# Optimization experiments

Measured on AMD Instinct MI355X. Metric: run time of the kernel, lower is better.

## Reference

```python
import jax, jax.numpy as jnp
import numpy as np

B, T, F, H = 16, 1024, 1024, 16
D = F // H  # 64

def setup_inputs() -> dict:
    key = jax.random.key(0)
    k0, k1, k2 = jax.random.split(key, 3)
    return {
        "x": jax.random.normal(k0, (B, T, F), jnp.float32),
        "mask": jnp.zeros((B, 1, T, 1), jnp.float32),
        "W_attn": jax.random.normal(k1, (F, 3 * F), jnp.float32) * 0.02,
        "b_attn": jnp.zeros((3 * F,), jnp.float32),
        "W_proj": jax.random.normal(k2, (F, F), jnp.float32) * 0.02,
        "b_proj": jnp.zeros((F,), jnp.float32),
    }

def reference(x, mask, W_attn, b_attn, W_proj, b_proj):
    # qkv projection (Conv1D == linear with transposed weight layout)
    qkv = x @ W_attn + b_attn                       # [B,T,3F]
    q, k, v = jnp.split(qkv, 3, axis=-1)
    split = lambda t: t.reshape(B, T, H, D).transpose(0, 2, 1, 3)  # [B,H,T,D]
    q, k, v = split(q), split(k), split(v)
    # non-standard: contract over T -> [B,H,D,D] score matrix
    s = jnp.einsum('bhtd,bhte->bhde', q, k) / jnp.sqrt(jnp.float32(D))
    tril = jnp.tril(jnp.ones((D, D), bool))         # bias buffer sliced to DxD
    s = jnp.where(tril, s, jnp.float32(-10000.0))
    # second matmul with V (before softmax), scaled by dk^2
    w = jnp.einsum('bhde,bhte->bhtd', s, v) / (jnp.float32(D) ** 2)  # [B,H,T,D]
    w = jax.nn.softmax(w + mask, axis=-2)           # softmax over T (dim=-2)
    a = w * v                                        # elementwise, not weighted sum
    merge = lambda t: t.transpose(0, 2, 1, 3).reshape(B, T, F)
    a = merge(a) @ W_proj + b_proj                   # output projection
    return a, merge(w)
```

## Files before the change

kernel.cpp:

```cpp
#include <hip/hip_runtime.h>
#include <math.h>

namespace {
constexpr int B = 16, T = 1024, F = 1024, H = 16, D = 64;
constexpr int NT = B * T;
constexpr int QKV_COLS = 3 * F;

constexpr size_t XHI_OFF = 0;
constexpr size_t XLO_OFF = 33554432;
constexpr size_t WAH_OFF = 67108864;
constexpr size_t WVL_OFF = 73400320;
constexpr size_t QB_OFF  = 75497472;
constexpr size_t KB_OFF  = 109051904;
constexpr size_t SB_OFF  = 142606336;
constexpr size_t AB_OFF  = 146800640;
constexpr size_t WPB_OFF = 180355072;
constexpr size_t VB_OFF   = QB_OFF;
constexpr size_t WRAW_OFF = XHI_OFF;
constexpr size_t SP_OFF   = WVL_OFF;
}

typedef __attribute__((ext_vector_type(8))) __bf16 bf16x8;
typedef __attribute__((ext_vector_type(4))) float f32x4;

__device__ __forceinline__ unsigned short f2bf(float f) {
  unsigned u = __builtin_bit_cast(unsigned, f);
  u += 0x7FFFu + ((u >> 16) & 1u);
  return (unsigned short)(u >> 16);
}
__device__ __forceinline__ float bf2f(unsigned short s) {
  return __builtin_bit_cast(float, (unsigned)s << 16);
}
__device__ __forceinline__ void gld16(const unsigned short* g, unsigned short* l) {
  __builtin_amdgcn_global_load_lds(
      (const __attribute__((address_space(1))) unsigned int*)g,
      (__attribute__((address_space(3))) unsigned int*)l, 16, 0, 0);
}

__global__ __launch_bounds__(256) void cast_x(const float* __restrict__ x,
                                              unsigned short* __restrict__ xhi,
                                              unsigned short* __restrict__ xlo) {
  int i = (blockIdx.x * 256 + threadIdx.x) * 4;
  float4 v = *(const float4*)&x[i];
  ushort4 h, l;
  h.x = f2bf(v.x); l.x = f2bf(v.x - bf2f(h.x));
  h.y = f2bf(v.y); l.y = f2bf(v.y - bf2f(h.y));
  h.z = f2bf(v.z); l.z = f2bf(v.z - bf2f(h.z));
  h.w = f2bf(v.w); l.w = f2bf(v.w - bf2f(h.w));
  *(ushort4*)&xhi[i] = h;
  *(ushort4*)&xlo[i] = l;
}

__global__ __launch_bounds__(256) void tcast(const float* __restrict__ W,
                                             unsigned short* __restrict__ Wt,
                                             unsigned short* __restrict__ Wlo,
                                             int ncols, int locol0) {
  __shared__ float tile[64][65];
  const int bx = blockIdx.x, by = blockIdx.y, tid = threadIdx.x;
#pragma unroll
  for (int i = 0; i < 16; ++i) {
    int idx = tid + i * 256;
    int r = idx >> 6, c = idx & 63;
    tile[r][c] = W[(size_t)(by * 64 + r) * ncols + bx * 64 + c];
  }
  __syncthreads();
#pragma unroll
  for (int i = 0; i < 16; ++i) {
    int idx = tid + i * 256;
    int r = idx >> 6, c = idx & 63;
    int col = bx * 64 + r;
    float w = tile[c][r];
    unsigned short h = f2bf(w);
    Wt[(size_t)col * 1024 + by * 64 + c] = h;
    if (col >= locol0) {
      Wlo[(size_t)(col - locol0) * 1024 + by * 64 + c] = f2bf(w - bf2f(h));
    }
  }
}

__device__ __forceinline__ void stage256(const unsigned short* __restrict__ Ag,
                                         const unsigned short* __restrict__ Bg,
                                         int row0, int col0, int kin,
                                         unsigned short* lbase, int wave,
                                         int lane) {
  const int rsub = lane >> 3;
  const int logb = ((lane & 7) ^ rsub) << 4;
  const int isB = logb >> 6;
  const int koff = kin + ((logb & 63) >> 1);
#pragma unroll
  for (int L = 0; L < 4; ++L) {
    const int R0 = (L * 8 + wave) * 8;
    const int r = R0 + rsub;
    const unsigned short* src =
        isB ? (Bg + (size_t)(col0 + r) * 1024 + koff)
            : (Ag + (size_t)(row0 + r) * 1024 + koff);
    gld16(src, lbase + (size_t)R0 * 64);
  }
}

template <int MODE>
__device__ __forceinline__ void tile_src(
    int kt, const unsigned short* __restrict__ A0,
    const unsigned short* __restrict__ A1,
    const unsigned short* __restrict__ B0,
    const unsigned short* __restrict__ B1,
    const unsigned short*& Ag, const unsigned short*& Bg, int& kin) {
  if constexpr (MODE == 1) {
    const int seg = kt >> 5;
    kin = (kt & 31) << 5;
    Ag = (seg == 1) ? A1 : A0;
    Bg = (seg == 2) ? B1 : B0;
  } else {
    Ag = A0; Bg = B0; kin = kt << 5;
  }
}

template <int MODE>
__global__ __launch_bounds__(512, 2) void gemm256(
    const unsigned short* __restrict__ A0, const unsigned short* __restrict__ A1,
    const unsigned short* __restrict__ B0, const unsigned short* __restrict__ B1,
    const float* __restrict__ bias, void* __restrict__ out0,
    void* __restrict__ out1) {
  __shared__ __align__(16) unsigned short lds[4][256][64];
  const int tid = threadIdx.x;
  const int wave = tid >> 6, lane = tid & 63;
  const int wr = wave >> 2, wc = wave & 3;
  const int m16 = lane & 15, quad = lane >> 4;
  const int row0 = blockIdx.y * 256, col0 = blockIdx.x * 256;
  constexpr int NKT = (MODE == 1) ? 96 : 32;
  f32x4 acc[8][4] = {};

#pragma unroll
  for (int p = 0; p < 3; ++p) {
    const unsigned short *Ag, *Bg; int kin;
    tile_src<MODE>(p, A0, A1, B0, B1, Ag, Bg, kin);
    stage256(Ag, Bg, row0, col0, kin, &lds[p][0][0], wave, lane);
  }

  for (int kt = 0; kt < NKT; ++kt) {
    if (kt + 3 < NKT) {
      const unsigned short *Ag, *Bg; int kin;
      tile_src<MODE>(kt + 3, A0, A1, B0, B1, Ag, Bg, kin);
      stage256(Ag, Bg, row0, col0, kin, &lds[(kt + 3) & 3][0][0], wave, lane);
      asm volatile("s_waitcnt vmcnt(12)" ::: "memory");
    } else {
      const int rem = NKT - 1 - kt;
      if (rem == 2)      asm volatile("s_waitcnt vmcnt(8)" ::: "memory");
      else if (rem == 1) asm volatile("s_waitcnt vmcnt(4)" ::: "memory");
      else               asm volatile("s_waitcnt vmcnt(0)" ::: "memory");
    }
    __builtin_amdgcn_s_barrier();
    __builtin_amdgcn_sched_barrier(0);

    const char* tb = (const char*)&lds[kt & 3][0][0];
    bf16x8 bfr[4], af0[4], af1[4];
#pragma unroll
    for (int j = 0; j < 4; ++j) {
      const int c = wc * 64 + j * 16 + m16;
      bfr[j] = *(const bf16x8*)(tb + c * 128 +
                                ((64 + quad * 16) ^ ((c & 7) << 4)));
    }
#pragma unroll
    for (int i = 0; i < 4; ++i) {
      const int r = wr * 128 + i * 16 + m16;
      af0[i] = *(const bf16x8*)(tb + r * 128 +
                                ((quad * 16) ^ ((r & 7) << 4)));
    }
#pragma unroll
    for (int i = 0; i < 4; ++i) {
      const int r = wr * 128 + 64 + i * 16 + m16;
      af1[i] = *(const bf16x8*)(tb + r * 128 +
                                ((quad * 16) ^ ((r & 7) << 4)));
    }
    __builtin_amdgcn_s_setprio(1);
#pragma unroll
    for (int i = 0; i < 4; ++i)
#pragma unroll
      for (int j = 0; j < 4; ++j)
        acc[i][j] = __builtin_amdgcn_mfma_f32_16x16x32_bf16(
            af0[i], bfr[j], acc[i][j], 0, 0, 0);
#pragma unroll
    for (int i = 0; i < 4; ++i)
#pragma unroll
      for (int j = 0; j < 4; ++j)
        acc[4 + i][j] = __builtin_amdgcn_mfma_f32_16x16x32_bf16(
            af1[i], bfr[j], acc[4 + i][j], 0, 0, 0);
    __builtin_amdgcn_s_setprio(0);
    __builtin_amdgcn_s_barrier();
    __builtin_amdgcn_sched_barrier(0);
  }

  if constexpr (MODE == 0) {
    unsigned short* dst = (col0 >= 1024) ? (unsigned short*)out1
                                         : (unsigned short*)out0;
#pragma unroll
    for (int j = 0; j < 4; ++j) {
      const int gcol = col0 + wc * 64 + j * 16 + m16;
      const int f = gcol & 1023;
      const int h = f >> 6, dd = f & 63;
      const float bv = bias[gcol];
#pragma unroll
      for (int i = 0; i < 8; ++i) {
#pragma unroll
        for (int r = 0; r < 4; ++r) {
          const int grow = row0 + wr * 128 + i * 16 + quad * 4 + r;
          const int b = grow >> 10, t = grow & 1023;
          dst[(((size_t)b * H + h) * T + t) * D + dd] = f2bf(acc[i][j][r] + bv);
        }
      }
    }
  } else if constexpr (MODE == 1) {
    float* vbp = (float*)out0;
#pragma unroll
    for (int j = 0; j < 4; ++j) {
      const int f = col0 + wc * 64 + j * 16 + m16;
      const int h = f >> 6, dd = f & 63;
      const float bv = bias[f];
#pragma unroll
      for (int i = 0; i < 8; ++i) {
#pragma unroll
        for (int r = 0; r < 4; ++r) {
          const int grow = row0 + wr * 128 + i * 16 + quad * 4 + r;
          const int b = grow >> 10, t = grow & 1023;
          vbp[(((size_t)b * H + h) * T + t) * D + dd] = acc[i][j][r] + bv;
        }
      }
    }
  } else {
    float* o = (float*)out0;
#pragma unroll
    for (int j = 0; j < 4; ++j) {
      const int gcol = col0 + wc * 64 + j * 16 + m16;
      const float bv = bias[gcol];
#pragma unroll
      for (int i = 0; i < 8; ++i) {
#pragma unroll
        for (int r = 0; r < 4; ++r) {
          const int grow = row0 + wr * 128 + i * 16 + quad * 4 + r;
          o[(size_t)grow * F + gcol] = acc[i][j][r] + bv;
        }
      }
    }
  }
}

__global__ __launch_bounds__(256) void score_kernel(
    const unsigned short* __restrict__ qb, const unsigned short* __restrict__ kb,
    float* __restrict__ sb) {
  __shared__ float qs[64][65];
  __shared__ float ks[64][65];
  const int bh = blockIdx.x;
  const int tid = threadIdx.x;
  const size_t base = (size_t)bh * T * D;
  const int d0 = (tid >> 4) * 4, e0 = (tid & 15) * 4;
  float acc[4][4] = {};
  for (int ch = 0; ch < T / 64; ++ch) {
#pragma unroll
    for (int i = 0; i < 4; ++i) {
      int idx = (tid + i * 256) * 4;
      ushort4 qv = *(const ushort4*)&qb[base + (size_t)ch * 4096 + idx];
      ushort4 kv = *(const ushort4*)&kb[base + (size_t)ch * 4096 + idx];
      int r = idx >> 6, c = idx & 63;
      qs[r][c] = bf2f(qv.x); qs[r][c+1] = bf2f(qv.y);
      qs[r][c+2] = bf2f(qv.z); qs[r][c+3] = bf2f(qv.w);
      ks[r][c] = bf2f(kv.x); ks[r][c+1] = bf2f(kv.y);
      ks[r][c+2] = bf2f(kv.z); ks[r][c+3] = bf2f(kv.w);
    }
    __syncthreads();
#pragma unroll 8
    for (int tt = 0; tt < 64; ++tt) {
      float qa[4], kv[4];
#pragma unroll
      for (int i = 0; i < 4; ++i) qa[i] = qs[tt][d0 + i];
#pragma unroll
      for (int j = 0; j < 4; ++j) kv[j] = ks[tt][e0 + j];
#pragma unroll
      for (int i = 0; i < 4; ++i)
#pragma unroll
        for (int j = 0; j < 4; ++j) acc[i][j] += qa[i] * kv[j];
    }
    __syncthreads();
  }
#pragma unroll
  for (int i = 0; i < 4; ++i) {
#pragma unroll
    for (int j = 0; j < 4; ++j) {
      int dd = d0 + i, ee = e0 + j;
      float v = acc[i][j] * 0.125f;
      if (ee > dd) v = -10000.0f;
      sb[(size_t)bh * (D * D) + dd * D + ee] = v;
    }
  }
}

__global__ __launch_bounds__(256) void exp_kernel(
    const float* __restrict__ vb, const float* __restrict__ sb,
    const float* __restrict__ mask, float* __restrict__ wraw,
    float* __restrict__ sp) {
  const int tc = blockIdx.x, bh = blockIdx.y;
  const int b = bh >> 4;
  const int tid = threadIdx.x;
  const int lane = tid & 63;
  const int dg = __builtin_amdgcn_readfirstlane(tid >> 6);
  const int tg = tc * 64 + lane;
  const float* vrow = vb + (size_t)bh * (T * D) + (size_t)tg * D;
  float4 vreg[16];
#pragma unroll
  for (int i = 0; i < 16; ++i) vreg[i] = *(const float4*)&vrow[i * 4];
  const float mval = mask[(size_t)b * T + tg];
  float ex[16];
#pragma unroll
  for (int dd = 0; dd < 16; ++dd) {
    const int d = dg * 16 + dd;
    const float* srow = sb + (size_t)bh * 4096 + (size_t)d * 64;
    float acc = 0.f;
#pragma unroll
    for (int e4 = 0; e4 < 16; ++e4) {
      float4 s4 = *(const float4*)&srow[e4 * 4];
      acc += s4.x * vreg[e4].x + s4.y * vreg[e4].y +
             s4.z * vreg[e4].z + s4.w * vreg[e4].w;
    }
    float w = acc * (1.0f / 4096.0f) + mval;
    ex[dd] = __expf(w);
    wraw[(size_t)bh * (T * D) + (size_t)d * T + tg] = ex[dd];
  }
#pragma unroll
  for (int dd = 0; dd < 16; ++dd) {
    float v = ex[dd];
    v += __shfl_xor(v, 1, 64);
    v += __shfl_xor(v, 2, 64);
    v += __shfl_xor(v, 4, 64);
    v += __shfl_xor(v, 8, 64);
    v += __shfl_xor(v, 16, 64);
    v += __shfl_xor(v, 32, 64);
    if (lane == 0) sp[((size_t)bh * 16 + tc) * 64 + dg * 16 + dd] = v;
  }
}

__global__ __launch_bounds__(256) void norm_kernel(
    const float* __restrict__ vb, const float* __restrict__ wraw,
    const float* __restrict__ sp, unsigned short* __restrict__ ab,
    float* __restrict__ out2) {
  __shared__ float wt[64][65];
  __shared__ float invS[64];
  const int tc = blockIdx.x, bh = blockIdx.y;
  const int b = bh >> 4, h = bh & 15;
  const int tid = threadIdx.x;
  if (tid < 64) {
    float S = 0.f;
#pragma unroll
    for (int j = 0; j < 16; ++j) S += sp[((size_t)bh * 16 + j) * 64 + tid];
    invS[tid] = 1.0f / S;
  }
#pragma unroll
  for (int i = 0; i < 16; ++i) {
    int idx = tid + i * 256;
    int dd = idx >> 6, tt = idx & 63;
    wt[dd][tt] = wraw[(size_t)bh * (T * D) + (size_t)dd * T + tc * 64 + tt];
  }
  __syncthreads();
  const int d = tid & 63, trow = tid >> 6;
#pragma unroll
  for (int j = 0; j < 16; ++j) {
    int tl = trow * 16 + j;
    int tg = tc * 64 + tl;
    float o = wt[d][tl] * invS[d];
    float vv = vb[(size_t)bh * (T * D) + (size_t)tg * D + d];
    size_t oidx = ((size_t)b * T + tg) * F + h * 64 + d;
    out2[oidx] = o;
    ab[oidx] = f2bf(o * vv);
  }
}

extern "C" void kernel_launch(void* const* d_in, const int* in_sizes, int n_in,
                              void* d_out, int out_size, void* d_ws,
                              size_t ws_size, hipStream_t stream) {
  const float* x = (const float*)d_in[0];
  const float* mask = (const float*)d_in[1];
  const float* Wa = (const float*)d_in[2];
  const float* ba = (const float*)d_in[3];
  const float* Wp = (const float*)d_in[4];
  const float* bp = (const float*)d_in[5];
  char* ws = (char*)d_ws;
  float* out = (float*)d_out;

  unsigned short* xhi = (unsigned short*)(ws + XHI_OFF);
  unsigned short* xlo = (unsigned short*)(ws + XLO_OFF);
  unsigned short* Wah = (unsigned short*)(ws + WAH_OFF);
  unsigned short* Wvl = (unsigned short*)(ws + WVL_OFF);
  unsigned short* qb  = (unsigned short*)(ws + QB_OFF);
  unsigned short* kb  = (unsigned short*)(ws + KB_OFF);
  float* sb   = (float*)(ws + SB_OFF);
  unsigned short* ab  = (unsigned short*)(ws + AB_OFF);
  unsigned short* Wpb = (unsigned short*)(ws + WPB_OFF);
  float* vb   = (float*)(ws + VB_OFF);
  float* wraw = (float*)(ws + WRAW_OFF);
  float* sp   = (float*)(ws + SP_OFF);

  cast_x<<<NT * F / 1024, 256, 0, stream>>>(x, xhi, xlo);
  tcast<<<dim3(QKV_COLS / 64, F / 64), 256, 0, stream>>>(Wa, Wah, Wvl,
                                                         QKV_COLS, 2048);
  tcast<<<dim3(F / 64, F / 64), 256, 0, stream>>>(Wp, Wpb, Wvl, F, 1 << 30);

  gemm256<0><<<dim3(2048 / 256, NT / 256), 512, 0, stream>>>(
      xhi, nullptr, Wah, nullptr, ba, qb, kb);

  score_kernel<<<dim3(B * H), 256, 0, stream>>>(qb, kb, sb);

  gemm256<1><<<dim3(F / 256, NT / 256), 512, 0, stream>>>(
      xhi, xlo, Wah + (size_t)2048 * 1024, Wvl, ba + 2048, vb, nullptr);

  exp_kernel<<<dim3(T / 64, B * H), 256, 0, stream>>>(vb, sb, mask, wraw, sp);

  norm_kernel<<<dim3(T / 64, B * H), 256, 0, stream>>>(
      vb, wraw, sp, ab, out + (size_t)NT * F);

  gemm256<2><<<dim3(F / 256, NT / 256), 512, 0, stream>>>(
      ab, nullptr, Wpb, nullptr, bp, out, nullptr);
}
```

Baseline: 630.3 us.

## Double-buffer LDS fragment reads in register to overlap with MFMA

Restructures the GEMM main loop so the LDS fragments for the next k-tile are read into a second register set while the MFMAs for the current tile run, ping-ponging between two fragment arrays. The loop is unrolled by two, with a peeled tail that adjusts the vmcnt waits. The aim is to hide LDS read latency behind matrix-core work. In exchange it holds 12 extra bf16x8 registers per thread, which under launch_bounds(512,2) may raise register pressure or cause spills.

```diff
diff --git a/kernel.cpp b/kernel.cpp
--- a/kernel.cpp
+++ b/kernel.cpp
@@ -115,6 +115,57 @@
   }
 }
 
+__device__ __forceinline__ void read_frags(const char* tb, int wr, int wc,
+                                           int m16, int quad,
+                                           bf16x8 (&dst)[12]) {
+#pragma unroll
+  for (int j = 0; j < 4; ++j) {
+    const int c = wc * 64 + j * 16 + m16;
+    dst[j] = *(const bf16x8*)(tb + c * 128 +
+                              ((64 + quad * 16) ^ ((c & 7) << 4)));
+  }
+#pragma unroll
+  for (int i = 0; i < 8; ++i) {
+    const int r = wr * 128 + i * 16 + m16;
+    dst[4 + i] = *(const bf16x8*)(tb + r * 128 +
+                                  ((quad * 16) ^ ((r & 7) << 4)));
+  }
+}
+
+template <int MODE, int VM, bool STG, bool RDN>
+__device__ __forceinline__ void half_body(
+    int j, int row0, int col0, const unsigned short* __restrict__ A0,
+    const unsigned short* __restrict__ A1,
+    const unsigned short* __restrict__ B0,
+    const unsigned short* __restrict__ B1,
+    unsigned short (*lds)[256][64], int wave, int lane, int wr, int wc,
+    int m16, int quad, bf16x8 (&cur)[12], bf16x8 (&nxt)[12],
+    f32x4 (&acc)[8][4]) {
+  if constexpr (STG) {
+    const unsigned short *Ag, *Bg; int kin;
+    tile_src<MODE>(j + 3, A0, A1, B0, B1, Ag, Bg, kin);
+    stage256(Ag, Bg, row0, col0, kin, &lds[(j + 3) & 3][0][0], wave, lane);
+  }
+  if constexpr (VM == 8)      asm volatile("s_waitcnt vmcnt(8)" ::: "memory");
+  else if constexpr (VM == 4) asm volatile("s_waitcnt vmcnt(4)" ::: "memory");
+  else if constexpr (VM == 0) asm volatile("s_waitcnt vmcnt(0)" ::: "memory");
+  __builtin_amdgcn_s_barrier();
+  __builtin_amdgcn_sched_barrier(0);
+  if constexpr (RDN) {
+    read_frags((const char*)&lds[(j + 1) & 3][0][0], wr, wc, m16, quad, nxt);
+  }
+  __builtin_amdgcn_s_setprio(1);
+#pragma unroll
+  for (int i = 0; i < 8; ++i)
+#pragma unroll
+    for (int jj = 0; jj < 4; ++jj)
+      acc[i][jj] = __builtin_amdgcn_mfma_f32_16x16x32_bf16(
+          cur[4 + i], cur[jj], acc[i][jj], 0, 0, 0);
+  __builtin_amdgcn_s_setprio(0);
+  __builtin_amdgcn_s_barrier();
+  __builtin_amdgcn_sched_barrier(0);
+}
+
 template <int MODE>
 __global__ __launch_bounds__(512, 2) void gemm256(
     const unsigned short* __restrict__ A0, const unsigned short* __restrict__ A1,
@@ -129,6 +180,7 @@
   const int row0 = blockIdx.y * 256, col0 = blockIdx.x * 256;
   constexpr int NKT = (MODE == 1) ? 96 : 32;
   f32x4 acc[8][4] = {};
+  bf16x8 s0[12], s1[12];
 
 #pragma unroll
   for (int p = 0; p < 3; ++p) {
@@ -136,59 +188,26 @@
     tile_src<MODE>(p, A0, A1, B0, B1, Ag, Bg, kin);
     stage256(Ag, Bg, row0, col0, kin, &lds[p][0][0], wave, lane);
   }
-
-  for (int kt = 0; kt < NKT; ++kt) {
-    if (kt + 3 < NKT) {
-      const unsigned short *Ag, *Bg; int kin;
-      tile_src<MODE>(kt + 3, A0, A1, B0, B1, Ag, Bg, kin);
-      stage256(Ag, Bg, row0, col0, kin, &lds[(kt + 3) & 3][0][0], wave, lane);
-      asm volatile("s_waitcnt vmcnt(12)" ::: "memory");
-    } else {
-      const int rem = NKT - 1 - kt;
-      if (rem == 2)      asm volatile("s_waitcnt vmcnt(8)" ::: "memory");
-      else if (rem == 1) asm volatile("s_waitcnt vmcnt(4)" ::: "memory");
-      else               asm volatile("s_waitcnt vmcnt(0)" ::: "memory");
-    }
-    __builtin_amdgcn_s_barrier();
-    __builtin_amdgcn_sched_barrier(0);
-
-    const char* tb = (const char*)&lds[kt & 3][0][0];
-    bf16x8 bfr[4], af0[4], af1[4];
-#pragma unroll
-    for (int j = 0; j < 4; ++j) {
-      const int c = wc * 64 + j * 16 + m16;
-      bfr[j] = *(const bf16x8*)(tb + c * 128 +
-                                ((64 + quad * 16) ^ ((c & 7) << 4)));
-    }
-#pragma unroll
-    for (int i = 0; i < 4; ++i) {
-      const int r = wr * 128 + i * 16 + m16;
-      af0[i] = *(const bf16x8*)(tb + r * 128 +
-                                ((quad * 16) ^ ((r & 7) << 4)));
-    }
-#pragma unroll
-    for (int i = 0; i < 4; ++i) {
-      const int r = wr * 128 + 64 + i * 16 + m16;
-      af1[i] = *(const bf16x8*)(tb + r * 128 +
-                                ((quad * 16) ^ ((r & 7) << 4)));
-    }
-    __builtin_amdgcn_s_setprio(1);
-#pragma unroll
-    for (int i = 0; i < 4; ++i)
-#pragma unroll
-      for (int j = 0; j < 4; ++j)
-        acc[i][j] = __builtin_amdgcn_mfma_f32_16x16x32_bf16(
-            af0[i], bfr[j], acc[i][j], 0, 0, 0);
-#pragma unroll
-    for (int i = 0; i < 4; ++i)
-#pragma unroll
-      for (int j = 0; j < 4; ++j)
-        acc[4 + i][j] = __builtin_amdgcn_mfma_f32_16x16x32_bf16(
-            af1[i], bfr[j], acc[4 + i][j], 0, 0, 0);
-    __builtin_amdgcn_s_setprio(0);
-    __builtin_amdgcn_s_barrier();
-    __builtin_amdgcn_sched_barrier(0);
-  }
+  asm volatile("s_waitcnt vmcnt(8)" ::: "memory");
+  __builtin_amdgcn_s_barrier();
+  __builtin_amdgcn_sched_barrier(0);
+  read_frags((const char*)&lds[0][0][0], wr, wc, m16, quad, s0);
+
+  int kt = 0;
+  for (; kt + 5 < NKT; kt += 2) {
+    half_body<MODE, 8, true, true>(kt, row0, col0, A0, A1, B0, B1, lds, wave,
+                                   lane, wr, wc, m16, quad, s0, s1, acc);
+    half_body<MODE, 8, true, true>(kt + 1, row0, col0, A0, A1, B0, B1, lds,
+                                   wave, lane, wr, wc, m16, quad, s1, s0, acc);
+  }
+  half_body<MODE, 8, true, true>(NKT - 4, row0, col0, A0, A1, B0, B1, lds,
+                                 wave, lane, wr, wc, m16, quad, s0, s1, acc);
+  half_body<MODE, 4, false, true>(NKT - 3, row0, col0, A0, A1, B0, B1, lds,
+                                  wave, lane, wr, wc, m16, quad, s1, s0, acc);
+  half_body<MODE, 0, false, true>(NKT - 2, row0, col0, A0, A1, B0, B1, lds,
+                                  wave, lane, wr, wc, m16, quad, s0, s1, acc);
+  half_body<MODE, -1, false, false>(NKT - 1, row0, col0, A0, A1, B0, B1, lds,
+                                    wave, lane, wr, wc, m16, quad, s1, s0, acc);
 
   if constexpr (MODE == 0) {
     unsigned short* dst = (col0 >= 1024) ? (unsigned short*)out1
```

Result: no change. 636.6 us (+1.0%).

## Split GEMM main loop into two half-phases interleaving global loads with MFMA

Applied to the files above, without the earlier changes.

The GEMM k-loop is split into two phases per tile. Each phase issues half of the next tile's global-to-LDS loads, loads one half of the A fragments, and runs 16 MFMAs, with an extra barrier in between. This spreads the prefetch traffic across the compute and lowers register pressure for the A fragments. The vmcnt waits are retuned to match. In exchange it adds a barrier per iteration, and the explicit lgkmcnt(0) waits may serialize LDS reads against the MFMAs.

```diff
diff --git a/kernel.cpp b/kernel.cpp
--- a/kernel.cpp
+++ b/kernel.cpp
@@ -78,17 +78,16 @@
   }
 }
 
-__device__ __forceinline__ void stage256(const unsigned short* __restrict__ Ag,
-                                         const unsigned short* __restrict__ Bg,
-                                         int row0, int col0, int kin,
-                                         unsigned short* lbase, int wave,
-                                         int lane) {
+__device__ __forceinline__ void stage_half(
+    const unsigned short* __restrict__ Ag,
+    const unsigned short* __restrict__ Bg, int row0, int col0, int kin,
+    unsigned short* lbase, int wave, int lane, int h) {
   const int rsub = lane >> 3;
   const int logb = ((lane & 7) ^ rsub) << 4;
   const int isB = logb >> 6;
   const int koff = kin + ((logb & 63) >> 1);
 #pragma unroll
-  for (int L = 0; L < 4; ++L) {
+  for (int L = 2 * h; L < 2 * h + 2; ++L) {
     const int R0 = (L * 8 + wave) * 8;
     const int r = R0 + rsub;
     const unsigned short* src =
@@ -134,26 +133,29 @@
   for (int p = 0; p < 3; ++p) {
     const unsigned short *Ag, *Bg; int kin;
     tile_src<MODE>(p, A0, A1, B0, B1, Ag, Bg, kin);
-    stage256(Ag, Bg, row0, col0, kin, &lds[p][0][0], wave, lane);
+    stage_half(Ag, Bg, row0, col0, kin, &lds[p][0][0], wave, lane, 0);
+    stage_half(Ag, Bg, row0, col0, kin, &lds[p][0][0], wave, lane, 1);
   }
 
   for (int kt = 0; kt < NKT; ++kt) {
+    const char* tb = (const char*)&lds[kt & 3][0][0];
     if (kt + 3 < NKT) {
       const unsigned short *Ag, *Bg; int kin;
       tile_src<MODE>(kt + 3, A0, A1, B0, B1, Ag, Bg, kin);
-      stage256(Ag, Bg, row0, col0, kin, &lds[(kt + 3) & 3][0][0], wave, lane);
-      asm volatile("s_waitcnt vmcnt(12)" ::: "memory");
+      stage_half(Ag, Bg, row0, col0, kin, &lds[(kt + 3) & 3][0][0], wave,
+                 lane, 0);
+      asm volatile("s_waitcnt vmcnt(10)" ::: "memory");
+    } else if (kt == NKT - 3) {
+      asm volatile("s_waitcnt vmcnt(8)" ::: "memory");
+    } else if (kt == NKT - 2) {
+      asm volatile("s_waitcnt vmcnt(4)" ::: "memory");
     } else {
-      const int rem = NKT - 1 - kt;
-      if (rem == 2)      asm volatile("s_waitcnt vmcnt(8)" ::: "memory");
-      else if (rem == 1) asm volatile("s_waitcnt vmcnt(4)" ::: "memory");
-      else               asm volatile("s_waitcnt vmcnt(0)" ::: "memory");
+      asm volatile("s_waitcnt vmcnt(0)" ::: "memory");
     }
     __builtin_amdgcn_s_barrier();
     __builtin_amdgcn_sched_barrier(0);
 
-    const char* tb = (const char*)&lds[kt & 3][0][0];
-    bf16x8 bfr[4], af0[4], af1[4];
+    bf16x8 bfr[4], af[4];
 #pragma unroll
     for (int j = 0; j < 4; ++j) {
       const int c = wc * 64 + j * 16 + m16;
@@ -163,28 +165,44 @@
 #pragma unroll
     for (int i = 0; i < 4; ++i) {
       const int r = wr * 128 + i * 16 + m16;
-      af0[i] = *(const bf16x8*)(tb + r * 128 +
-                                ((quad * 16) ^ ((r & 7) << 4)));
-    }
+      af[i] = *(const bf16x8*)(tb + r * 128 +
+                               ((quad * 16) ^ ((r & 7) << 4)));
+    }
+    asm volatile("s_waitcnt lgkmcnt(0)" ::: "memory");
+    __builtin_amdgcn_sched_barrier(0);
+    __builtin_amdgcn_s_setprio(1);
+#pragma unroll
+    for (int i = 0; i < 4; ++i)
+#pragma unroll
+      for (int j = 0; j < 4; ++j)
+        acc[i][j] = __builtin_amdgcn_mfma_f32_16x16x32_bf16(
+            af[i], bfr[j], acc[i][j], 0, 0, 0);
+    __builtin_amdgcn_s_setprio(0);
+    __builtin_amdgcn_s_barrier();
+    __builtin_amdgcn_sched_barrier(0);
+
+    if (kt + 3 < NKT) {
+      const unsigned short *Ag, *Bg; int kin;
+      tile_src<MODE>(kt + 3, A0, A1, B0, B1, Ag, Bg, kin);
+      stage_half(Ag, Bg, row0, col0, kin, &lds[(kt + 3) & 3][0][0], wave,
+                 lane, 1);
+    }
+    bf16x8 af2[4];
 #pragma unroll
     for (int i = 0; i < 4; ++i) {
       const int r = wr * 128 + 64 + i * 16 + m16;
-      af1[i] = *(const bf16x8*)(tb + r * 128 +
+      af2[i] = *(const bf16x8*)(tb + r * 128 +
                                 ((quad * 16) ^ ((r & 7) << 4)));
     }
+    asm volatile("s_waitcnt lgkmcnt(0)" ::: "memory");
+    __builtin_amdgcn_sched_barrier(0);
     __builtin_amdgcn_s_setprio(1);
-#pragma unroll
-    for (int i = 0; i < 4; ++i)
-#pragma unroll
-      for (int j = 0; j < 4; ++j)
-        acc[i][j] = __builtin_amdgcn_mfma_f32_16x16x32_bf16(
-            af0[i], bfr[j], acc[i][j], 0, 0, 0);
 #pragma unroll
     for (int i = 0; i < 4; ++i)
 #pragma unroll
       for (int j = 0; j < 4; ++j)
         acc[4 + i][j] = __builtin_amdgcn_mfma_f32_16x16x32_bf16(
-            af1[i], bfr[j], acc[4 + i][j], 0, 0, 0);
+            af2[i], bfr[j], acc[4 + i][j], 0, 0, 0);
     __builtin_amdgcn_s_setprio(0);
     __builtin_amdgcn_s_barrier();
     __builtin_amdgcn_sched_barrier(0);
```

New measurement: 644.7 us. 2.3% more time.
